# Kernel optimization log

Measured on AMD Instinct MI355X. Metric: run time of the kernel, lower is better.

## Reference

```python
import jax, jax.numpy as jnp
import numpy as np

N, NU, R, NX, NY = 16384, 2, 256, 8, 2


def setup_inputs() -> dict:
    key = jax.random.key(0)
    ks = jax.random.split(key, 10)
    A = jax.random.normal(ks[0], (NX, NX), dtype=jnp.float32)
    # scale A to be stable (spectral radius < 1) so the 16k-step recurrence is well-behaved
    rho = jnp.max(jnp.abs(jnp.linalg.eigvals(A.astype(jnp.float32)))).real
    A = (A * (0.95 / rho)).astype(jnp.float32)
    return {
        "u": jax.random.normal(ks[1], (N, NU, R), dtype=jnp.float32),
        "x0": jax.random.normal(ks[2], (NX, R), dtype=jnp.float32),
        "A": A,
        "B_u": jax.random.normal(ks[3], (NX, NU), dtype=jnp.float32),
        "C_y": jax.random.normal(ks[4], (NY, NX), dtype=jnp.float32),
        "D_yu": jax.random.normal(ks[5], (NY, NU), dtype=jnp.float32),
        "u_mean": jax.random.normal(ks[6], (NU,), dtype=jnp.float32),
        "u_std": jax.random.uniform(ks[7], (NU,), dtype=jnp.float32, minval=0.5, maxval=1.5),
        "y_mean": jax.random.normal(ks[8], (NY,), dtype=jnp.float32),
        "y_std": jax.random.uniform(ks[9], (NY,), dtype=jnp.float32, minval=0.5, maxval=1.5),
    }


def reference(u, x0, A, B_u, C_y, D_yu, u_mean, u_std, y_mean, y_std):
    # normalize input as in _simulate_core
    un = (u - u_mean.reshape(1, -1, 1)) / u_std.reshape(1, -1, 1)  # (N, nu, R)

    def step(x, uk):
        # x: (nx, R), uk: (nu, R)
        y = C_y @ x + D_yu @ uk      # (ny, R)
        x_next = A @ x + B_u @ uk    # (nx, R)
        return x_next, (y, x)

    _, (Y, X) = jax.lax.scan(step, x0, un)  # Y: (N, ny, R), X: (N, nx, R)

    # denormalize output
    y = Y * y_std.reshape(1, -1, 1) + y_mean.reshape(1, -1, 1)
    return y, X
```

## Files before the change

### kernel.cpp

```cpp
#include <hip/hip_runtime.h>


#define NSTEPS 16384
#define NUI 2
#define RB 256
#define NXS 8
#define NYO 2
#define LF 32
#define NC1 (NSTEPS / LF)
#define NC2 (NC1 / 4)

__global__ void pow_k(const float* __restrict__ A, float* __restrict__ A32,
                      float* __restrict__ A64, float* __restrict__ A96,
                      float* __restrict__ A128) {
    __shared__ float M[64], T32[64];
    const int t = threadIdx.x;
    const int i = t >> 3, j = t & 7;
    M[t] = A[t];
    __syncthreads();
    for (int it = 0; it < 5; ++it) {
        float acc = 0.f;
        #pragma unroll
        for (int k = 0; k < 8; ++k) acc += M[i * 8 + k] * M[k * 8 + j];
        __syncthreads();
        M[t] = acc;
        __syncthreads();
    }
    T32[t] = M[t];
    A32[t] = M[t];
    {
        float acc = 0.f;
        #pragma unroll
        for (int k = 0; k < 8; ++k) acc += M[i * 8 + k] * M[k * 8 + j];
        __syncthreads();
        M[t] = acc;
        __syncthreads();
    }
    A64[t] = M[t];
    float a96 = 0.f, a128 = 0.f;
    #pragma unroll
    for (int k = 0; k < 8; ++k) {
        a96  += M[i * 8 + k] * T32[k * 8 + j];
        a128 += M[i * 8 + k] * M[k * 8 + j];
    }
    A96[t] = a96;
    A128[t] = a128;
}

__global__ __launch_bounds__(RB) void phase1_k(
    const float* __restrict__ u, const float* __restrict__ A,
    const float* __restrict__ Bu, const float* __restrict__ um,
    const float* __restrict__ us, float* __restrict__ d32) {
    const int c = blockIdx.x;
    const int r = threadIdx.x;
    float a[NXS][NXS];
    #pragma unroll
    for (int i = 0; i < NXS; ++i)
        #pragma unroll
        for (int j = 0; j < NXS; ++j) a[i][j] = A[i * NXS + j];
    float b0[NXS], b1[NXS];
    #pragma unroll
    for (int i = 0; i < NXS; ++i) { b0[i] = Bu[i * NUI]; b1[i] = Bu[i * NUI + 1]; }
    const float um0 = um[0], um1 = um[1];
    const float is0 = 1.0f / us[0], is1 = 1.0f / us[1];
    float t[NXS];
    #pragma unroll
    for (int i = 0; i < NXS; ++i) t[i] = 0.f;
    const float* up = u + (size_t)c * LF * NUI * RB + r;
    #pragma unroll 4
    for (int j = 0; j < LF; ++j) {
        const float u0 = (up[0]  - um0) * is0;
        const float u1 = (up[RB] - um1) * is1;
        up += NUI * RB;
        float nt[NXS];
        #pragma unroll
        for (int i = 0; i < NXS; ++i) {
            float acc = fmaf(b0[i], u0, b1[i] * u1);
            #pragma unroll
            for (int k = 0; k < NXS; ++k) acc = fmaf(a[i][k], t[k], acc);
            nt[i] = acc;
        }
        #pragma unroll
        for (int i = 0; i < NXS; ++i) t[i] = nt[i];
    }
    float* dp = d32 + (size_t)c * NXS * RB + r;
    #pragma unroll
    for (int i = 0; i < NXS; ++i) dp[i * RB] = t[i];
}

__global__ __launch_bounds__(RB) void combine4_k(
    const float* __restrict__ d32, const float* __restrict__ A32,
    const float* __restrict__ A64, const float* __restrict__ A96,
    float* __restrict__ d128) {
    const int m = blockIdx.x;
    const int r = threadIdx.x;
    float m32[NXS][NXS], m64[NXS][NXS], m96[NXS][NXS];
    #pragma unroll
    for (int i = 0; i < NXS; ++i)
        #pragma unroll
        for (int j = 0; j < NXS; ++j) {
            m32[i][j] = A32[i * NXS + j];
            m64[i][j] = A64[i * NXS + j];
            m96[i][j] = A96[i * NXS + j];
        }
    const float* p = d32 + (size_t)(4 * m) * NXS * RB + r;
    float x0[NXS], x1[NXS], x2[NXS], x3[NXS];
    #pragma unroll
    for (int i = 0; i < NXS; ++i) {
        x0[i] = p[i * RB];
        x1[i] = p[(size_t)NXS * RB + i * RB];
        x2[i] = p[(size_t)2 * NXS * RB + i * RB];
        x3[i] = p[(size_t)3 * NXS * RB + i * RB];
    }
    float* o = d128 + (size_t)m * NXS * RB + r;
    #pragma unroll
    for (int i = 0; i < NXS; ++i) {
        float acc = x3[i];
        #pragma unroll
        for (int k = 0; k < NXS; ++k) {
            acc = fmaf(m96[i][k], x0[k], acc);
            acc = fmaf(m64[i][k], x1[k], acc);
            acc = fmaf(m32[i][k], x2[k], acc);
        }
        o[i * RB] = acc;
    }
}

__global__ __launch_bounds__(64) void phase2_k(
    const float* __restrict__ x0, const float* __restrict__ A128,
    const float* __restrict__ d128, float* __restrict__ s128) {
    const int r = blockIdx.x * 64 + threadIdx.x;
    float m[NXS][NXS];
    #pragma unroll
    for (int i = 0; i < NXS; ++i)
        #pragma unroll
        for (int j = 0; j < NXS; ++j) m[i][j] = A128[i * NXS + j];
    float s[NXS];
    #pragma unroll
    for (int i = 0; i < NXS; ++i) s[i] = x0[i * RB + r];
    float P[8][NXS];
    #pragma unroll
    for (int sl = 0; sl < 8; ++sl) {
        const float* dp = d128 + (size_t)sl * NXS * RB + r;
        #pragma unroll
        for (int i = 0; i < NXS; ++i) P[sl][i] = dp[i * RB];
    }
    for (int c = 0; c < NC2; c += 8) {
        #pragma unroll
        for (int sl = 0; sl < 8; ++sl) {
            const int cc = c + sl;
            float* sp = s128 + (size_t)cc * NXS * RB + r;
            #pragma unroll
            for (int i = 0; i < NXS; ++i) sp[i * RB] = s[i];
            float ns[NXS];
            #pragma unroll
            for (int i = 0; i < NXS; ++i) {
                float acc = P[sl][i];
                #pragma unroll
                for (int k = 0; k < NXS; ++k) acc = fmaf(m[i][k], s[k], acc);
                ns[i] = acc;
            }
            if (cc + 8 < NC2) {
                const float* dp = d128 + (size_t)(cc + 8) * NXS * RB + r;
                #pragma unroll
                for (int i = 0; i < NXS; ++i) P[sl][i] = dp[i * RB];
            }
            #pragma unroll
            for (int i = 0; i < NXS; ++i) s[i] = ns[i];
        }
    }
}

__global__ __launch_bounds__(RB) void phase3_k(
    const float* __restrict__ u, const float* __restrict__ s128,
    const float* __restrict__ d32, const float* __restrict__ A32,
    const float* __restrict__ A, const float* __restrict__ Bu,
    const float* __restrict__ Cy, const float* __restrict__ Dyu,
    const float* __restrict__ um, const float* __restrict__ us,
    const float* __restrict__ ym, const float* __restrict__ ys,
    float* __restrict__ Y, float* __restrict__ X) {
    const int c = blockIdx.x;
    const int r = threadIdx.x;
    const int m = c >> 2;
    const int p = c & 3;
    float a[NXS][NXS];
    #pragma unroll
    for (int i = 0; i < NXS; ++i)
        #pragma unroll
        for (int j = 0; j < NXS; ++j) a[i][j] = A[i * NXS + j];
    float b0[NXS], b1[NXS], c0[NXS], c1[NXS];
    #pragma unroll
    for (int i = 0; i < NXS; ++i) { b0[i] = Bu[i * NUI]; b1[i] = Bu[i * NUI + 1]; }
    #pragma unroll
    for (int k = 0; k < NXS; ++k) { c0[k] = Cy[k]; c1[k] = Cy[NXS + k]; }
    const float d00 = Dyu[0], d01 = Dyu[1], d10 = Dyu[2], d11 = Dyu[3];
    const float um0 = um[0], um1 = um[1];
    const float is0 = 1.0f / us[0], is1 = 1.0f / us[1];
    const float ym0 = ym[0], ym1 = ym[1], ys0 = ys[0], ys1 = ys[1];

    float t[NXS];
    {
        const float* sp = s128 + (size_t)m * NXS * RB + r;
        #pragma unroll
        for (int i = 0; i < NXS; ++i) t[i] = sp[i * RB];
    }
    if (p) {
        float a32[NXS][NXS];
        #pragma unroll
        for (int i = 0; i < NXS; ++i)
            #pragma unroll
            for (int j = 0; j < NXS; ++j) a32[i][j] = A32[i * NXS + j];
        for (int q = 0; q < p; ++q) {
            const float* dp = d32 + (size_t)(4 * m + q) * NXS * RB + r;
            float nt[NXS];
            #pragma unroll
            for (int i = 0; i < NXS; ++i) {
                float acc = dp[i * RB];
                #pragma unroll
                for (int k = 0; k < NXS; ++k) acc = fmaf(a32[i][k], t[k], acc);
                nt[i] = acc;
            }
            #pragma unroll
            for (int i = 0; i < NXS; ++i) t[i] = nt[i];
        }
    }

    const float* up = u + (size_t)c * LF * NUI * RB + r;
    float* Xp = X + (size_t)c * LF * NXS * RB + r;
    float* Yp = Y + (size_t)c * LF * NYO * RB + r;
    #pragma unroll 4
    for (int j = 0; j < LF; ++j) {
        const float u0 = (up[0]  - um0) * is0;
        const float u1 = (up[RB] - um1) * is1;
        up += NUI * RB;
        #pragma unroll
        for (int i = 0; i < NXS; ++i)
            __builtin_nontemporal_store(t[i], Xp + i * RB);
        Xp += NXS * RB;
        float y0 = fmaf(d00, u0, d01 * u1);
        float y1 = fmaf(d10, u0, d11 * u1);
        #pragma unroll
        for (int k = 0; k < NXS; ++k) {
            y0 = fmaf(c0[k], t[k], y0);
            y1 = fmaf(c1[k], t[k], y1);
        }
        __builtin_nontemporal_store(fmaf(y0, ys0, ym0), Yp);
        __builtin_nontemporal_store(fmaf(y1, ys1, ym1), Yp + RB);
        Yp += NYO * RB;
        float nt[NXS];
        #pragma unroll
        for (int i = 0; i < NXS; ++i) {
            float acc = fmaf(b0[i], u0, b1[i] * u1);
            #pragma unroll
            for (int k = 0; k < NXS; ++k) acc = fmaf(a[i][k], t[k], acc);
            nt[i] = acc;
        }
        #pragma unroll
        for (int i = 0; i < NXS; ++i) t[i] = nt[i];
    }
}

extern "C" void kernel_launch(void* const* d_in, const int* in_sizes, int n_in,
                              void* d_out, int out_size, void* d_ws, size_t ws_size,
                              hipStream_t stream) {
    const float* u   = (const float*)d_in[0];
    const float* x0  = (const float*)d_in[1];
    const float* A   = (const float*)d_in[2];
    const float* Bu  = (const float*)d_in[3];
    const float* Cy  = (const float*)d_in[4];
    const float* Dyu = (const float*)d_in[5];
    const float* um  = (const float*)d_in[6];
    const float* us  = (const float*)d_in[7];
    const float* ym  = (const float*)d_in[8];
    const float* ys  = (const float*)d_in[9];

    float* Y = (float*)d_out;
    float* X = Y + (size_t)NSTEPS * NYO * RB;

    float* ws   = (float*)d_ws;
    float* A32  = ws;
    float* A64  = ws + 64;
    float* A96  = ws + 128;
    float* A128 = ws + 192;
    float* d32  = ws + 256;
    float* d128 = d32 + (size_t)NC1 * NXS * RB;
    float* s128 = d128 + (size_t)NC2 * NXS * RB;

    pow_k<<<1, 64, 0, stream>>>(A, A32, A64, A96, A128);
    phase1_k<<<NC1, RB, 0, stream>>>(u, A, Bu, um, us, d32);
    combine4_k<<<NC2, RB, 0, stream>>>(d32, A32, A64, A96, d128);
    phase2_k<<<4, 64, 0, stream>>>(x0, A128, d128, s128);
    phase3_k<<<NC1, RB, 0, stream>>>(u, s128, d32, A32, A, Bu, Cy, Dyu,
                                     um, us, ym, ys, Y, X);
}
```

Before: 255.5 us.

## Fuse all scan phases into one persistent kernel with hierarchical grid barriers

```diff
diff --git a/kernel.cpp b/kernel.cpp
--- a/kernel.cpp
+++ b/kernel.cpp
@@ -9,254 +9,271 @@
 #define LF 32
 #define NC1 (NSTEPS / LF)
 #define NC2 (NC1 / 4)
-
-__global__ void pow_k(const float* __restrict__ A, float* __restrict__ A32,
-                      float* __restrict__ A64, float* __restrict__ A96,
-                      float* __restrict__ A128) {
-    __shared__ float M[64], T32[64];
-    const int t = threadIdx.x;
-    const int i = t >> 3, j = t & 7;
-    M[t] = A[t];
+#define NBLK NC1
+#define GRPSH 5
+#define NGRP (NBLK >> GRPSH)
+
+__device__ __forceinline__ void grid_sync(unsigned* bar, int bid, unsigned phase) {
     __syncthreads();
-    for (int it = 0; it < 5; ++it) {
-        float acc = 0.f;
-        #pragma unroll
-        for (int k = 0; k < 8; ++k) acc += M[i * 8 + k] * M[k * 8 + j];
-        __syncthreads();
-        M[t] = acc;
-        __syncthreads();
-    }
-    T32[t] = M[t];
-    A32[t] = M[t];
-    {
-        float acc = 0.f;
-        #pragma unroll
-        for (int k = 0; k < 8; ++k) acc += M[i * 8 + k] * M[k * 8 + j];
-        __syncthreads();
-        M[t] = acc;
-        __syncthreads();
-    }
-    A64[t] = M[t];
-    float a96 = 0.f, a128 = 0.f;
-    #pragma unroll
-    for (int k = 0; k < 8; ++k) {
-        a96  += M[i * 8 + k] * T32[k * 8 + j];
-        a128 += M[i * 8 + k] * M[k * 8 + j];
-    }
-    A96[t] = a96;
-    A128[t] = a128;
+    if (threadIdx.x == 0) {
+        __threadfence();
+        unsigned* grp  = bar + ((bid >> GRPSH) << 5);
+        unsigned* root = bar + (NGRP << 5);
+        unsigned o = __hip_atomic_fetch_add(grp, 1u, __ATOMIC_RELAXED,
+                                            __HIP_MEMORY_SCOPE_AGENT);
+        if ((o & 31u) == 31u)
+            __hip_atomic_fetch_add(root, 1u, __ATOMIC_RELAXED,
+                                   __HIP_MEMORY_SCOPE_AGENT);
+        const unsigned tgt = phase * (unsigned)NGRP;
+        while (__hip_atomic_load(root, __ATOMIC_RELAXED,
+                                 __HIP_MEMORY_SCOPE_AGENT) < tgt)
+            __builtin_amdgcn_s_sleep(1);
+        __threadfence();
+    }
+    __syncthreads();
 }
 
-__global__ __launch_bounds__(RB) void phase1_k(
-    const float* __restrict__ u, const float* __restrict__ A,
-    const float* __restrict__ Bu, const float* __restrict__ um,
-    const float* __restrict__ us, float* __restrict__ d32) {
-    const int c = blockIdx.x;
-    const int r = threadIdx.x;
-    float a[NXS][NXS];
-    #pragma unroll
-    for (int i = 0; i < NXS; ++i)
-        #pragma unroll
-        for (int j = 0; j < NXS; ++j) a[i][j] = A[i * NXS + j];
-    float b0[NXS], b1[NXS];
-    #pragma unroll
-    for (int i = 0; i < NXS; ++i) { b0[i] = Bu[i * NUI]; b1[i] = Bu[i * NUI + 1]; }
-    const float um0 = um[0], um1 = um[1];
-    const float is0 = 1.0f / us[0], is1 = 1.0f / us[1];
-    float t[NXS];
-    #pragma unroll
-    for (int i = 0; i < NXS; ++i) t[i] = 0.f;
-    const float* up = u + (size_t)c * LF * NUI * RB + r;
-    #pragma unroll 4
-    for (int j = 0; j < LF; ++j) {
-        const float u0 = (up[0]  - um0) * is0;
-        const float u1 = (up[RB] - um1) * is1;
-        up += NUI * RB;
-        float nt[NXS];
-        #pragma unroll
-        for (int i = 0; i < NXS; ++i) {
-            float acc = fmaf(b0[i], u0, b1[i] * u1);
-            #pragma unroll
-            for (int k = 0; k < NXS; ++k) acc = fmaf(a[i][k], t[k], acc);
-            nt[i] = acc;
-        }
-        #pragma unroll
-        for (int i = 0; i < NXS; ++i) t[i] = nt[i];
-    }
-    float* dp = d32 + (size_t)c * NXS * RB + r;
-    #pragma unroll
-    for (int i = 0; i < NXS; ++i) dp[i * RB] = t[i];
-}
-
-__global__ __launch_bounds__(RB) void combine4_k(
-    const float* __restrict__ d32, const float* __restrict__ A32,
-    const float* __restrict__ A64, const float* __restrict__ A96,
-    float* __restrict__ d128) {
-    const int m = blockIdx.x;
-    const int r = threadIdx.x;
-    float m32[NXS][NXS], m64[NXS][NXS], m96[NXS][NXS];
-    #pragma unroll
-    for (int i = 0; i < NXS; ++i)
-        #pragma unroll
-        for (int j = 0; j < NXS; ++j) {
-            m32[i][j] = A32[i * NXS + j];
-            m64[i][j] = A64[i * NXS + j];
-            m96[i][j] = A96[i * NXS + j];
-        }
-    const float* p = d32 + (size_t)(4 * m) * NXS * RB + r;
-    float x0[NXS], x1[NXS], x2[NXS], x3[NXS];
-    #pragma unroll
-    for (int i = 0; i < NXS; ++i) {
-        x0[i] = p[i * RB];
-        x1[i] = p[(size_t)NXS * RB + i * RB];
-        x2[i] = p[(size_t)2 * NXS * RB + i * RB];
-        x3[i] = p[(size_t)3 * NXS * RB + i * RB];
-    }
-    float* o = d128 + (size_t)m * NXS * RB + r;
-    #pragma unroll
-    for (int i = 0; i < NXS; ++i) {
-        float acc = x3[i];
-        #pragma unroll
-        for (int k = 0; k < NXS; ++k) {
-            acc = fmaf(m96[i][k], x0[k], acc);
-            acc = fmaf(m64[i][k], x1[k], acc);
-            acc = fmaf(m32[i][k], x2[k], acc);
-        }
-        o[i * RB] = acc;
-    }
-}
-
-__global__ __launch_bounds__(64) void phase2_k(
-    const float* __restrict__ x0, const float* __restrict__ A128,
-    const float* __restrict__ d128, float* __restrict__ s128) {
-    const int r = blockIdx.x * 64 + threadIdx.x;
-    float m[NXS][NXS];
-    #pragma unroll
-    for (int i = 0; i < NXS; ++i)
-        #pragma unroll
-        for (int j = 0; j < NXS; ++j) m[i][j] = A128[i * NXS + j];
-    float s[NXS];
-    #pragma unroll
-    for (int i = 0; i < NXS; ++i) s[i] = x0[i * RB + r];
-    float P[8][NXS];
-    #pragma unroll
-    for (int sl = 0; sl < 8; ++sl) {
-        const float* dp = d128 + (size_t)sl * NXS * RB + r;
-        #pragma unroll
-        for (int i = 0; i < NXS; ++i) P[sl][i] = dp[i * RB];
-    }
-    for (int c = 0; c < NC2; c += 8) {
-        #pragma unroll
-        for (int sl = 0; sl < 8; ++sl) {
-            const int cc = c + sl;
-            float* sp = s128 + (size_t)cc * NXS * RB + r;
-            #pragma unroll
-            for (int i = 0; i < NXS; ++i) sp[i * RB] = s[i];
-            float ns[NXS];
-            #pragma unroll
-            for (int i = 0; i < NXS; ++i) {
-                float acc = P[sl][i];
-                #pragma unroll
-                for (int k = 0; k < NXS; ++k) acc = fmaf(m[i][k], s[k], acc);
-                ns[i] = acc;
-            }
-            if (cc + 8 < NC2) {
-                const float* dp = d128 + (size_t)(cc + 8) * NXS * RB + r;
-                #pragma unroll
-                for (int i = 0; i < NXS; ++i) P[sl][i] = dp[i * RB];
-            }
-            #pragma unroll
-            for (int i = 0; i < NXS; ++i) s[i] = ns[i];
-        }
-    }
-}
-
-__global__ __launch_bounds__(RB) void phase3_k(
-    const float* __restrict__ u, const float* __restrict__ s128,
-    const float* __restrict__ d32, const float* __restrict__ A32,
+__global__ __launch_bounds__(256, 2) void fused_scan_k(
+    const float* __restrict__ u, const float* __restrict__ x0,
     const float* __restrict__ A, const float* __restrict__ Bu,
     const float* __restrict__ Cy, const float* __restrict__ Dyu,
     const float* __restrict__ um, const float* __restrict__ us,
     const float* __restrict__ ym, const float* __restrict__ ys,
-    float* __restrict__ Y, float* __restrict__ X) {
+    float* __restrict__ Y, float* __restrict__ X,
+    float* __restrict__ d32, float* __restrict__ d128,
+    float* __restrict__ s128, unsigned* __restrict__ bar) {
+    __shared__ float P32[64], P64[64], P96[64], P128[64], Mt[64];
+    const int tid = threadIdx.x;
     const int c = blockIdx.x;
-    const int r = threadIdx.x;
-    const int m = c >> 2;
-    const int p = c & 3;
-    float a[NXS][NXS];
-    #pragma unroll
-    for (int i = 0; i < NXS; ++i)
-        #pragma unroll
-        for (int j = 0; j < NXS; ++j) a[i][j] = A[i * NXS + j];
-    float b0[NXS], b1[NXS], c0[NXS], c1[NXS];
-    #pragma unroll
-    for (int i = 0; i < NXS; ++i) { b0[i] = Bu[i * NUI]; b1[i] = Bu[i * NUI + 1]; }
-    #pragma unroll
-    for (int k = 0; k < NXS; ++k) { c0[k] = Cy[k]; c1[k] = Cy[NXS + k]; }
-    const float d00 = Dyu[0], d01 = Dyu[1], d10 = Dyu[2], d11 = Dyu[3];
+    const int li = tid >> 3, lj = tid & 7;
+
+    if (tid < 64) Mt[tid] = A[tid];
+    __syncthreads();
+    for (int it = 0; it < 5; ++it) {
+        float acc = 0.f;
+        if (tid < 64) {
+            #pragma unroll
+            for (int k = 0; k < 8; ++k) acc += Mt[li * 8 + k] * Mt[k * 8 + lj];
+        }
+        __syncthreads();
+        if (tid < 64) Mt[tid] = acc;
+        __syncthreads();
+    }
+    if (tid < 64) P32[tid] = Mt[tid];
+    {
+        float acc = 0.f;
+        if (tid < 64) {
+            #pragma unroll
+            for (int k = 0; k < 8; ++k) acc += Mt[li * 8 + k] * Mt[k * 8 + lj];
+        }
+        __syncthreads();
+        if (tid < 64) Mt[tid] = acc;
+        __syncthreads();
+    }
+    if (tid < 64) {
+        float a96 = 0.f, a128 = 0.f;
+        #pragma unroll
+        for (int k = 0; k < 8; ++k) {
+            a96  += Mt[li * 8 + k] * P32[k * 8 + lj];
+            a128 += Mt[li * 8 + k] * Mt[k * 8 + lj];
+        }
+        P64[tid] = Mt[tid];
+        P96[tid] = a96;
+        P128[tid] = a128;
+    }
+    __syncthreads();
+
     const float um0 = um[0], um1 = um[1];
     const float is0 = 1.0f / us[0], is1 = 1.0f / us[1];
-    const float ym0 = ym[0], ym1 = ym[1], ys0 = ys[0], ys1 = ys[1];
-
-    float t[NXS];
+
     {
-        const float* sp = s128 + (size_t)m * NXS * RB + r;
-        #pragma unroll
-        for (int i = 0; i < NXS; ++i) t[i] = sp[i * RB];
-    }
-    if (p) {
-        float a32[NXS][NXS];
+        float a[NXS][NXS];
         #pragma unroll
         for (int i = 0; i < NXS; ++i)
             #pragma unroll
-            for (int j = 0; j < NXS; ++j) a32[i][j] = A32[i * NXS + j];
+            for (int j = 0; j < NXS; ++j) a[i][j] = A[i * NXS + j];
+        float b0[NXS], b1[NXS];
+        #pragma unroll
+        for (int i = 0; i < NXS; ++i) {
+            b0[i] = Bu[i * NUI];
+            b1[i] = Bu[i * NUI + 1];
+        }
+        float t[NXS];
+        #pragma unroll
+        for (int i = 0; i < NXS; ++i) t[i] = 0.f;
+        const float* up = u + (size_t)c * LF * NUI * RB + tid;
+        #pragma unroll 4
+        for (int j = 0; j < LF; ++j) {
+            const float u0 = (up[0]  - um0) * is0;
+            const float u1 = (up[RB] - um1) * is1;
+            up += NUI * RB;
+            float nt[NXS];
+            #pragma unroll
+            for (int i = 0; i < NXS; ++i) {
+                float acc = fmaf(b0[i], u0, b1[i] * u1);
+                #pragma unroll
+                for (int k = 0; k < NXS; ++k) acc = fmaf(a[i][k], t[k], acc);
+                nt[i] = acc;
+            }
+            #pragma unroll
+            for (int i = 0; i < NXS; ++i) t[i] = nt[i];
+        }
+        float* dp = d32 + (size_t)c * NXS * RB + tid;
+        #pragma unroll
+        for (int i = 0; i < NXS; ++i) dp[i * RB] = t[i];
+    }
+
+    grid_sync(bar, c, 1u);
+
+    if (c < NC2) {
+        const float* p = d32 + (size_t)(4 * c) * NXS * RB + tid;
+        float x0v[NXS], x1v[NXS], x2v[NXS], x3v[NXS];
+        #pragma unroll
+        for (int i = 0; i < NXS; ++i) {
+            x0v[i] = p[i * RB];
+            x1v[i] = p[(size_t)NXS * RB + i * RB];
+            x2v[i] = p[(size_t)2 * NXS * RB + i * RB];
+            x3v[i] = p[(size_t)3 * NXS * RB + i * RB];
+        }
+        float* o = d128 + (size_t)c * NXS * RB + tid;
+        #pragma unroll
+        for (int i = 0; i < NXS; ++i) {
+            float acc = x3v[i];
+            #pragma unroll
+            for (int k = 0; k < NXS; ++k) {
+                acc = fmaf(P96[i * 8 + k], x0v[k], acc);
+                acc = fmaf(P64[i * 8 + k], x1v[k], acc);
+                acc = fmaf(P32[i * 8 + k], x2v[k], acc);
+            }
+            o[i * RB] = acc;
+        }
+    }
+
+    grid_sync(bar, c, 2u);
+
+    if (c == 0) {
+        float m[NXS][NXS];
+        #pragma unroll
+        for (int i = 0; i < NXS; ++i)
+            #pragma unroll
+            for (int j = 0; j < NXS; ++j) m[i][j] = P128[i * 8 + j];
+        float s[NXS];
+        #pragma unroll
+        for (int i = 0; i < NXS; ++i) s[i] = x0[i * RB + tid];
+        float P[4][NXS];
+        #pragma unroll
+        for (int sl = 0; sl < 4; ++sl) {
+            const float* dp = d128 + (size_t)sl * NXS * RB + tid;
+            #pragma unroll
+            for (int i = 0; i < NXS; ++i) P[sl][i] = dp[i * RB];
+        }
+        for (int it = 0; it < NC2; it += 4) {
+            #pragma unroll
+            for (int sl = 0; sl < 4; ++sl) {
+                const int cc = it + sl;
+                float* sp = s128 + (size_t)cc * NXS * RB + tid;
+                #pragma unroll
+                for (int i = 0; i < NXS; ++i) sp[i * RB] = s[i];
+                float d[NXS];
+                #pragma unroll
+                for (int i = 0; i < NXS; ++i) d[i] = P[sl][i];
+                if (cc + 4 < NC2) {
+                    const float* dp = d128 + (size_t)(cc + 4) * NXS * RB + tid;
+                    #pragma unroll
+                    for (int i = 0; i < NXS; ++i) P[sl][i] = dp[i * RB];
+                }
+                float ns[NXS];
+                #pragma unroll
+                for (int i = 0; i < NXS; ++i) {
+                    float acc = d[i];
+                    #pragma unroll
+                    for (int k = 0; k < NXS; ++k) acc = fmaf(m[i][k], s[k], acc);
+                    ns[i] = acc;
+                }
+                #pragma unroll
+                for (int i = 0; i < NXS; ++i) s[i] = ns[i];
+            }
+        }
+    }
+
+    grid_sync(bar, c, 3u);
+
+    {
+        const int mm = c >> 2;
+        const int p = c & 3;
+        float t[NXS];
+        {
+            const float* sp = s128 + (size_t)mm * NXS * RB + tid;
+            #pragma unroll
+            for (int i = 0; i < NXS; ++i) t[i] = sp[i * RB];
+        }
         for (int q = 0; q < p; ++q) {
-            const float* dp = d32 + (size_t)(4 * m + q) * NXS * RB + r;
+            const float* dp = d32 + (size_t)(4 * mm + q) * NXS * RB + tid;
             float nt[NXS];
             #pragma unroll
             for (int i = 0; i < NXS; ++i) {
                 float acc = dp[i * RB];
                 #pragma unroll
-                for (int k = 0; k < NXS; ++k) acc = fmaf(a32[i][k], t[k], acc);
+                for (int k = 0; k < NXS; ++k)
+                    acc = fmaf(P32[i * 8 + k], t[k], acc);
                 nt[i] = acc;
             }
             #pragma unroll
             for (int i = 0; i < NXS; ++i) t[i] = nt[i];
         }
-    }
-
-    const float* up = u + (size_t)c * LF * NUI * RB + r;
-    float* Xp = X + (size_t)c * LF * NXS * RB + r;
-    float* Yp = Y + (size_t)c * LF * NYO * RB + r;
-    #pragma unroll 4
-    for (int j = 0; j < LF; ++j) {
-        const float u0 = (up[0]  - um0) * is0;
-        const float u1 = (up[RB] - um1) * is1;
-        up += NUI * RB;
+
+        float a[NXS][NXS];
         #pragma unroll
         for (int i = 0; i < NXS; ++i)
-            __builtin_nontemporal_store(t[i], Xp + i * RB);
-        Xp += NXS * RB;
-        float y0 = fmaf(d00, u0, d01 * u1);
-        float y1 = fmaf(d10, u0, d11 * u1);
+            #pragma unroll
+            for (int j = 0; j < NXS; ++j) a[i][j] = A[i * NXS + j];
+        float b0[NXS], b1[NXS], c0[NXS], c1[NXS];
+        #pragma unroll
+        for (int i = 0; i < NXS; ++i) {
+            b0[i] = Bu[i * NUI];
+            b1[i] = Bu[i * NUI + 1];
+        }
         #pragma unroll
         for (int k = 0; k < NXS; ++k) {
-            y0 = fmaf(c0[k], t[k], y0);
-            y1 = fmaf(c1[k], t[k], y1);
-        }
-        __builtin_nontemporal_store(fmaf(y0, ys0, ym0), Yp);
-        __builtin_nontemporal_store(fmaf(y1, ys1, ym1), Yp + RB);
-        Yp += NYO * RB;
-        float nt[NXS];
-        #pragma unroll
-        for (int i = 0; i < NXS; ++i) {
-            float acc = fmaf(b0[i], u0, b1[i] * u1);
-            #pragma unroll
-            for (int k = 0; k < NXS; ++k) acc = fmaf(a[i][k], t[k], acc);
-            nt[i] = acc;
-        }
-        #pragma unroll
-        for (int i = 0; i < NXS; ++i) t[i] = nt[i];
+            c0[k] = Cy[k];
+            c1[k] = Cy[NXS + k];
+        }
+        const float d00 = Dyu[0], d01 = Dyu[1], d10 = Dyu[2], d11 = Dyu[3];
+        const float ym0 = ym[0], ym1 = ym[1], ys0 = ys[0], ys1 = ys[1];
+
+        const float* up = u + (size_t)c * LF * NUI * RB + tid;
+        float* Xp = X + (size_t)c * LF * NXS * RB + tid;
+        float* Yp = Y + (size_t)c * LF * NYO * RB + tid;
+        #pragma unroll 4
+        for (int j = 0; j < LF; ++j) {
+            const float u0 = (up[0]  - um0) * is0;
+            const float u1 = (up[RB] - um1) * is1;
+            up += NUI * RB;
+            #pragma unroll
+            for (int i = 0; i < NXS; ++i)
+                __builtin_nontemporal_store(t[i], Xp + i * RB);
+            Xp += NXS * RB;
+            float y0 = fmaf(d00, u0, d01 * u1);
+            float y1 = fmaf(d10, u0, d11 * u1);
+            #pragma unroll
+            for (int k = 0; k < NXS; ++k) {
+                y0 = fmaf(c0[k], t[k], y0);
+                y1 = fmaf(c1[k], t[k], y1);
+            }
+            __builtin_nontemporal_store(fmaf(y0, ys0, ym0), Yp);
+            __builtin_nontemporal_store(fmaf(y1, ys1, ym1), Yp + RB);
+            Yp += NYO * RB;
+            float nt[NXS];
+            #pragma unroll
+            for (int i = 0; i < NXS; ++i) {
+                float acc = fmaf(b0[i], u0, b1[i] * u1);
+                #pragma unroll
+                for (int k = 0; k < NXS; ++k) acc = fmaf(a[i][k], t[k], acc);
+                nt[i] = acc;
+            }
+            #pragma unroll
+            for (int i = 0; i < NXS; ++i) t[i] = nt[i];
+        }
     }
 }
 
@@ -278,18 +295,12 @@
     float* X = Y + (size_t)NSTEPS * NYO * RB;
 
     float* ws   = (float*)d_ws;
-    float* A32  = ws;
-    float* A64  = ws + 64;
-    float* A96  = ws + 128;
-    float* A128 = ws + 192;
-    float* d32  = ws + 256;
+    float* d32  = ws;
     float* d128 = d32 + (size_t)NC1 * NXS * RB;
     float* s128 = d128 + (size_t)NC2 * NXS * RB;
-
-    pow_k<<<1, 64, 0, stream>>>(A, A32, A64, A96, A128);
-    phase1_k<<<NC1, RB, 0, stream>>>(u, A, Bu, um, us, d32);
-    combine4_k<<<NC2, RB, 0, stream>>>(d32, A32, A64, A96, d128);
-    phase2_k<<<4, 64, 0, stream>>>(x0, A128, d128, s128);
-    phase3_k<<<NC1, RB, 0, stream>>>(u, s128, d32, A32, A, Bu, Cy, Dyu,
-                                     um, us, ym, ys, Y, X);
+    unsigned* bar = (unsigned*)(s128 + (size_t)NC2 * NXS * RB);
+
+    hipMemsetAsync(bar, 0, (NGRP + 1) * 32 * sizeof(unsigned), stream);
+    fused_scan_k<<<NBLK, 256, 0, stream>>>(u, x0, A, Bu, Cy, Dyu, um, us, ym, ys,
+                                           Y, X, d32, d128, s128, bar);
 }
```

Result: slower. 317.0 us (+24.1%).
